# Kernel optimization log

Measured on AMD Instinct MI355X. Metric: run time of the kernel, lower is better.

Reference implementation:

```python
import jax, jax.numpy as jnp
import numpy as np

EPS = 1e-5

def bn(x, g, b, m, v):
    # inference-mode BatchNorm2d over channel dim
    return (x - m[None, :, None, None]) * jax.lax.rsqrt(v[None, :, None, None] + EPS) * g[None, :, None, None] + b[None, :, None, None]

def conv1x1(x, W, b=None):
    y = jnp.einsum('oc,bchw->bohw', W, x)
    return y + b[None, :, None, None] if b is not None else y

def forward(x, W3, b3, g1, b1, m1, v1, Wa, ba, g2, b2, m2, v2, Wq, bq, Wk, bk, Wv, bv, gam, Wg, bg, g3, b3n, m3, v3, Wf, bf, g4, b4, m4, v4, Wr, rs):
    B, C, H, Wd = x.shape
    N = H * Wd
    # conv branch: 3x3 conv + BN + ReLU
    y3 = jax.lax.conv_general_dilated(x, W3, (1, 1), ((1, 1), (1, 1)), dimension_numbers=('NCHW', 'OIHW', 'NCHW'))
    local = jax.nn.relu(bn(y3 + b3[None, :, None, None], g1, b1, m1, v1))
    # attn branch: 1x1 conv + BN + ReLU, then full-resolution attention
    a = jax.nn.relu(bn(conv1x1(x, Wa, ba), g2, b2, m2, v2))
    q = conv1x1(a, Wq, bq).reshape(B, -1, N)   # [B, C/8, N]
    k = conv1x1(a, Wk, bk).reshape(B, -1, N)   # [B, C/8, N]
    v = conv1x1(a, Wv, bv).reshape(B, -1, N)   # [B, C, N]
    att = jax.nn.softmax(jnp.einsum('bcn,bcm->bnm', q, k), axis=-1)  # [B, N, N], unscaled as in source
    o = jnp.einsum('bcm,bnm->bcn', v, att).reshape(a.shape)
    attn_feat = gam * o + a
    # gated fusion
    combined = jnp.concatenate([local, attn_feat], axis=1)
    gate = jax.nn.sigmoid(bn(conv1x1(combined, Wg, bg), g3, b3n, m3, v3))
    fused = gate * local + (1.0 - gate) * attn_feat
    out = jax.nn.relu(bn(conv1x1(jnp.concatenate([fused, combined], axis=1), Wf, bf), g4, b4, m4, v4))
    res = conv1x1(x, Wr)  # residual 1x1 conv, no bias (in != out channels)
    return out + rs * res

def setup_inputs() -> dict:
    B, Ci, Co, H, W_ = 4, 64, 128, 64, 64
    Cq = Co // 8
    ks = jax.random.split(jax.random.key(0), 24)
    def rn(i, s, sc=0.05):
        return jax.random.normal(ks[i], s, jnp.float32) * sc
    def var(i, c):
        return jax.random.uniform(ks[i], (c,), jnp.float32, 0.5, 1.5)
    ones = lambda c: jnp.ones((c,), jnp.float32)
    zeros = lambda c: jnp.zeros((c,), jnp.float32)
    return {
        'x': rn(0, (B, Ci, H, W_), 1.0),
        'W3': rn(1, (Co, Ci, 3, 3)), 'b3': rn(2, (Co,)),
        'g1': ones(Co), 'b1': zeros(Co), 'm1': rn(3, (Co,), 0.1), 'v1': var(4, Co),
        'Wa': rn(5, (Co, Ci)), 'ba': rn(6, (Co,)),
        'g2': ones(Co), 'b2': zeros(Co), 'm2': rn(7, (Co,), 0.1), 'v2': var(8, Co),
        'Wq': rn(9, (Cq, Co)), 'bq': rn(10, (Cq,)),
        'Wk': rn(11, (Cq, Co)), 'bk': rn(12, (Cq,)),
        'Wv': rn(13, (Co, Co)), 'bv': rn(14, (Co,)),
        'gam': jnp.array(0.5, jnp.float32),
        'Wg': rn(15, (Co, 2 * Co)), 'bg': rn(16, (Co,)),
        'g3': ones(Co), 'b3n': zeros(Co), 'm3': rn(17, (Co,), 0.1), 'v3': var(18, Co),
        'Wf': rn(19, (Co, 3 * Co)), 'bf': rn(20, (Co,)),
        'g4': ones(Co), 'b4': zeros(Co), 'm4': rn(21, (Co,), 0.1), 'v4': var(22, Co),
        'Wr': rn(23, (Co, Ci)),
        'rs': jnp.array(0.1, jnp.float32),
    }

def reference(x, W3, b3, g1, b1, m1, v1, Wa, ba, g2, b2, m2, v2, Wq, bq, Wk, bk, Wv, bv, gam, Wg, bg, g3, b3n, m3, v3, Wf, bf, g4, b4, m4, v4, Wr, rs):
    return forward(x, W3, b3, g1, b1, m1, v1, Wa, ba, g2, b2, m2, v2, Wq, bq, Wk, bk, Wv, bv, gam, Wg, bg, g3, b3n, m3, v3, Wf, bf, g4, b4, m4, v4, Wr, rs)
```

## Files before the change

### kernel.cpp

```cpp
#include <hip/hip_runtime.h>
#include <hip/hip_bf16.h>

#define CI_ 64
#define CO_ 128
#define NPIX 4096
#define CQ_ 16
#define EPS_ 1e-5f

typedef __attribute__((ext_vector_type(8))) __bf16 bf16x8;
typedef __attribute__((ext_vector_type(4))) __bf16 bf16x4;
typedef __attribute__((ext_vector_type(4))) float f32x4;

__global__ __launch_bounds__(256) void z_prepx(
    const float* __restrict__ x, __bf16* __restrict__ xT)
{
    __shared__ float tl[64][65];
    int b = blockIdx.x >> 6;
    int n0 = (blockIdx.x & 63) * 64;
    int tid = threadIdx.x;
    int nn = tid & 63, c4 = tid >> 6;
#pragma unroll
    for (int p = 0; p < 16; ++p) {
        int ci = p * 4 + c4;
        tl[ci][nn] = x[((size_t)b * CI_ + ci) * NPIX + n0 + nn];
    }
    __syncthreads();
#pragma unroll
    for (int p = 0; p < 2; ++p) {
        int idx = p * 256 + tid;
        int n = idx >> 3, cig = idx & 7;
        bf16x8 vv;
#pragma unroll
        for (int j = 0; j < 8; ++j) vv[j] = (__bf16)tl[cig * 8 + j][n];
        ((bf16x8*)xT)[((size_t)b * NPIX + n0 + n) * 8 + cig] = vv;
    }
}

__global__ __launch_bounds__(256) void z_prepw2(
    const float* __restrict__ W3, __bf16* __restrict__ Wt2,
    const float* __restrict__ Wg, const float* __restrict__ Wf, const float* __restrict__ Wr,
    const float* __restrict__ Wa, const float* __restrict__ Wq, const float* __restrict__ Wk,
    const float* __restrict__ Wv, __bf16* __restrict__ Wb)
{
    int i = blockIdx.x * 256 + threadIdx.x;
    if (i < 73728) {
        int co = i / 576;
        int r = i - co * 576;
        int tap = r >> 6;
        int ci = r & 63;
        Wt2[i] = (__bf16)W3[((size_t)co * CI_ + ci) * 9 + tap];
    }
    if (i < 118784) {
        float val;
        if (i < 32768) val = Wg[i];
        else if (i < 81920) val = Wf[i - 32768];
        else if (i < 90112) val = Wr[i - 81920];
        else if (i < 98304) val = Wa[i - 90112];
        else if (i < 100352) val = Wq[i - 98304];
        else if (i < 102400) val = Wk[i - 100352];
        else val = Wv[i - 102400];
        Wb[i] = (__bf16)val;
    }
}

__global__ __launch_bounds__(256) void z_mega(
    const __bf16* __restrict__ xT, const __bf16* __restrict__ Wb,
    const float* __restrict__ ba, const float* __restrict__ g2, const float* __restrict__ b2,
    const float* __restrict__ m2, const float* __restrict__ v2,
    const float* __restrict__ bq, const float* __restrict__ bk, const float* __restrict__ bv,
    float* __restrict__ a, float* __restrict__ q, __bf16* __restrict__ kT, __bf16* __restrict__ V2)
{
    __shared__ __align__(16) __bf16 an[16 * 128];
    int tid = threadIdx.x;
    int b = blockIdx.x >> 8;
    int n0 = (blockIdx.x & 255) * 16;
    int l = tid & 63, w = tid >> 6;
    int lm = l & 15, g = l >> 4;

    const __bf16* Wa2 = Wb + 90112;
    const __bf16* Wq2 = Wb + 98304;
    const __bf16* Wk2 = Wb + 100352;
    const __bf16* Wv2 = Wb + 102400;

    bf16x8 bx[2];
#pragma unroll
    for (int kc = 0; kc < 2; ++kc)
        bx[kc] = ((const bf16x8*)xT)[((size_t)b * NPIX + n0 + lm) * 8 + (kc * 4 + g)];
    f32x4 pa[2];
#pragma unroll
    for (int ct = 0; ct < 2; ++ct) {
#pragma unroll
        for (int r = 0; r < 4; ++r) pa[ct][r] = ba[w * 32 + ct * 16 + g * 4 + r];
#pragma unroll
        for (int kc = 0; kc < 2; ++kc) {
            bf16x8 afr = *(const bf16x8*)&Wa2[(size_t)(w * 32 + ct * 16 + lm) * 64 + kc * 32 + g * 8];
            pa[ct] = __builtin_amdgcn_mfma_f32_16x16x32_bf16(afr, bx[kc], pa[ct], 0, 0, 0);
        }
    }
#pragma unroll
    for (int ct = 0; ct < 2; ++ct) {
        bf16x4 pk;
#pragma unroll
        for (int r = 0; r < 4; ++r) {
            int co = w * 32 + ct * 16 + g * 4 + r;
            float sc = rsqrtf(v2[co] + EPS_) * g2[co];
            float sh = b2[co] - m2[co] * sc;
            float y = fmaxf(pa[ct][r] * sc + sh, 0.f);
            a[((size_t)b * CO_ + co) * NPIX + n0 + lm] = y;
            pk[r] = (__bf16)y;
        }
        int co8 = w * 4 + ct * 2 + (g >> 1);
        int ch = co8 ^ (lm & 7);
        *(bf16x4*)&an[lm * 128 + ch * 8 + (g & 1) * 4] = pk;
    }
    __syncthreads();

    bf16x8 bn[4];
#pragma unroll
    for (int kc = 0; kc < 4; ++kc) {
        int ch = (kc * 4 + g) ^ (lm & 7);
        bn[kc] = *(const bf16x8*)&an[lm * 128 + ch * 8];
    }
    f32x4 pv[2];
#pragma unroll
    for (int ct = 0; ct < 2; ++ct) {
#pragma unroll
        for (int r = 0; r < 4; ++r) pv[ct][r] = bv[w * 32 + ct * 16 + g * 4 + r];
#pragma unroll
        for (int kc = 0; kc < 4; ++kc) {
            bf16x8 afr = *(const bf16x8*)&Wv2[(size_t)(w * 32 + ct * 16 + lm) * 128 + kc * 32 + g * 8];
            pv[ct] = __builtin_amdgcn_mfma_f32_16x16x32_bf16(afr, bn[kc], pv[ct], 0, 0, 0);
        }
    }
    int n = n0 + lm;
#pragma unroll
    for (int ct = 0; ct < 2; ++ct)
#pragma unroll
        for (int r = 0; r < 4; ++r) {
            int c = w * 32 + ct * 16 + g * 4 + r;
            V2[(size_t)b * 524288 + (size_t)(n >> 3) * 1024 + c * 8 + (n & 7)] = (__bf16)pv[ct][r];
        }
    if (w == 0) {
        f32x4 pq;
#pragma unroll
        for (int r = 0; r < 4; ++r) pq[r] = bq[g * 4 + r];
#pragma unroll
        for (int kc = 0; kc < 4; ++kc) {
            bf16x8 afr = *(const bf16x8*)&Wq2[(size_t)lm * 128 + kc * 32 + g * 8];
            pq = __builtin_amdgcn_mfma_f32_16x16x32_bf16(afr, bn[kc], pq, 0, 0, 0);
        }
#pragma unroll
        for (int r = 0; r < 4; ++r)
            q[((size_t)b * CQ_ + g * 4 + r) * NPIX + n] = pq[r];
    } else if (w == 1) {
        f32x4 pk2;
#pragma unroll
        for (int r = 0; r < 4; ++r) pk2[r] = bk[g * 4 + r];
#pragma unroll
        for (int kc = 0; kc < 4; ++kc) {
            bf16x8 afr = *(const bf16x8*)&Wk2[(size_t)lm * 128 + kc * 32 + g * 8];
            pk2 = __builtin_amdgcn_mfma_f32_16x16x32_bf16(afr, bn[kc], pk2, 0, 0, 0);
        }
        bf16x4 kk;
#pragma unroll
        for (int r = 0; r < 4; ++r) kk[r] = (__bf16)pk2[r];
        *(bf16x4*)&kT[((size_t)b * NPIX + n) * CQ_ + g * 4] = kk;
    }
}

__global__ __launch_bounds__(256) void z_conv3m(
    const __bf16* __restrict__ xT, const __bf16* __restrict__ Wt2,
    const float* __restrict__ b3, const float* __restrict__ g,
    const float* __restrict__ bb, const float* __restrict__ m,
    const float* __restrict__ v, float* __restrict__ local)
{
    __shared__ __align__(16) __bf16 xt[3 * 66 * 64];
    __shared__ __align__(16) __bf16 wt[32 * 576];
    __shared__ float scs[32], shs[32];

    int blk = blockIdx.x;
    int b = blk >> 8;
    int h = (blk >> 2) & 63;
    int cg = blk & 3;
    int co0 = cg * 32;
    int tid = threadIdx.x;
    int l = tid & 63;
    int nt = tid >> 6;
    int lm = l & 15, lh = l >> 4;

    if (tid < 32) {
        int co = co0 + tid;
        float scv = rsqrtf(v[co] + EPS_) * g[co];
        scs[tid] = scv;
        shs[tid] = (b3[co] - m[co]) * scv + bb[co];
    }

    const bf16x8* xs = (const bf16x8*)xT + (size_t)b * (NPIX * 8);
    for (int i = tid; i < 1584; i += 256) {
        int r = i / 528;
        int rem = i - r * 528;
        int c = rem >> 3;
        int cig = rem & 7;
        int hh = h + r - 1;
        int gc = c - 1;
        bf16x8 val;
#pragma unroll
        for (int j = 0; j < 8; ++j) val[j] = (__bf16)0.f;
        if ((unsigned)hh < 64u && (unsigned)gc < 64u)
            val = xs[(hh * 64 + gc) * 8 + cig];
        *(bf16x8*)&xt[(r * 66 + c) * 64 + ((cig ^ (c & 7)) * 8)] = val;
    }
    const bf16x8* wsrc = (const bf16x8*)Wt2 + (size_t)co0 * 72;
    for (int i = tid; i < 2304; i += 256) {
        int co = i / 72;
        int kc = i - co * 72;
        *(bf16x8*)&wt[co * 576 + ((kc ^ (co & 7)) * 8)] = wsrc[i];
    }
    __syncthreads();

    f32x4 acc0 = {0.f, 0.f, 0.f, 0.f};
    f32x4 acc1 = {0.f, 0.f, 0.f, 0.f};
#pragma unroll
    for (int tap = 0; tap < 9; ++tap) {
        int dh = tap / 3, dw = tap % 3;
#pragma unroll
        for (int ks = 0; ks < 2; ++ks) {
            int cig = ks * 4 + lh;
            int col = nt * 16 + lm + dw;
            bf16x8 bfr = *(const bf16x8*)&xt[(dh * 66 + col) * 64 + ((cig ^ (col & 7)) * 8)];
            int kcg = tap * 8 + cig;
            bf16x8 a0 = *(const bf16x8*)&wt[lm * 576 + ((kcg ^ (lm & 7)) * 8)];
            bf16x8 a1 = *(const bf16x8*)&wt[(16 + lm) * 576 + ((kcg ^ (lm & 7)) * 8)];
            acc0 = __builtin_amdgcn_mfma_f32_16x16x32_bf16(a0, bfr, acc0, 0, 0, 0);
            acc1 = __builtin_amdgcn_mfma_f32_16x16x32_bf16(a1, bfr, acc1, 0, 0, 0);
        }
    }

    size_t obase = (size_t)b * CO_ * NPIX + h * 64 + nt * 16 + lm;
#pragma unroll
    for (int r = 0; r < 4; ++r) {
        int cl0 = lh * 4 + r;
        float y0 = fmaxf(acc0[r] * scs[cl0] + shs[cl0], 0.f);
        local[obase + (size_t)(co0 + cl0) * NPIX] = y0;
        int cl1 = 16 + cl0;
        float y1 = fmaxf(acc1[r] * scs[cl1] + shs[cl1], 0.f);
        local[obase + (size_t)(co0 + cl1) * NPIX] = y1;
    }
}

__global__ __launch_bounds__(256) void z_attn8(
    const float* __restrict__ q, const __bf16* __restrict__ kT, const __bf16* __restrict__ V2,
    __bf16* __restrict__ o_part, float2* __restrict__ ml)
{
    __shared__ __align__(16) unsigned char smem[16896];
    __shared__ float wmaxA[4][16], wsumA[4][16], fsA[16];
    __shared__ float wmaxB[4][16], wsumB[4][16], fsB[16];
    __bf16* pA = (__bf16*)smem;
    __bf16* pB = (__bf16*)(smem + 8448);
    float* o_lds = (float*)smem;

    int tid = threadIdx.x;
    int b = blockIdx.x >> 8;
    int half = (blockIdx.x >> 7) & 1;
    int q0 = (blockIdx.x & 127) * 32;
    int l = tid & 63;
    int w = tid >> 6;
    int lm = l & 15;
    int g = l >> 4;

    bf16x8 qfA, qfB;
#pragma unroll
    for (int j = 0; j < 8; ++j) { qfA[j] = (__bf16)0.f; qfB[j] = (__bf16)0.f; }
    if (g < 2) {
#pragma unroll
        for (int j = 0; j < 8; ++j) {
            qfA[j] = (__bf16)q[((size_t)b * CQ_ + g * 8 + j) * NPIX + q0 + lm];
            qfB[j] = (__bf16)q[((size_t)b * CQ_ + g * 8 + j) * NPIX + q0 + 16 + lm];
        }
    }

    float mA = -1e30f, lA = 0.f, mB = -1e30f, lB = 0.f;
    f32x4 aA0 = {0.f,0.f,0.f,0.f}, aA1 = {0.f,0.f,0.f,0.f};
    f32x4 aB0 = {0.f,0.f,0.f,0.f}, aB1 = {0.f,0.f,0.f,0.f};
    int c0 = w * 32 + lm;
    int c1 = c0 + 16;
    const bf16x8* vbase = (const bf16x8*)V2 + (size_t)b * 65536;
    const __bf16* ktb = kT + (size_t)b * NPIX * CQ_;

    for (int t = 0; t < 8; ++t) {
        int m0 = half * 2048 + t * 256;
        {
            f32x4 sfr[4];
#pragma unroll
            for (int ms = 0; ms < 4; ++ms) {
                bf16x8 kf;
#pragma unroll
                for (int j = 0; j < 8; ++j) kf[j] = (__bf16)0.f;
                if (g < 2)
                    kf = *(const bf16x8*)&ktb[(size_t)(m0 + w * 64 + ms * 16 + lm) * CQ_ + g * 8];
                f32x4 zz = {0.f, 0.f, 0.f, 0.f};
                sfr[ms] = __builtin_amdgcn_mfma_f32_16x16x32_bf16(kf, qfA, zz, 0, 0, 0);
            }
            float pmax = -1e30f;
#pragma unroll
            for (int ms = 0; ms < 4; ++ms)
#pragma unroll
                for (int r = 0; r < 4; ++r) pmax = fmaxf(pmax, sfr[ms][r]);
            pmax = fmaxf(pmax, __shfl_xor(pmax, 16));
            pmax = fmaxf(pmax, __shfl_xor(pmax, 32));
            if (g == 0) wmaxA[w][lm] = pmax;
            __syncthreads();
            float tmax = fmaxf(fmaxf(wmaxA[0][lm], wmaxA[1][lm]), fmaxf(wmaxA[2][lm], wmaxA[3][lm]));
            float nm = fmaxf(mA, tmax);
            float f = __expf(mA - nm);
            mA = nm;
            if (w == 0 && g == 0) fsA[lm] = f;
            float psum = 0.f;
#pragma unroll
            for (int ms = 0; ms < 4; ++ms) {
                float p0 = __expf(sfr[ms][0] - nm);
                float p1 = __expf(sfr[ms][1] - nm);
                float p2 = __expf(sfr[ms][2] - nm);
                float p3 = __expf(sfr[ms][3] - nm);
                psum += (p0 + p1) + (p2 + p3);
                bf16x4 pk;
                pk[0] = (__bf16)p0; pk[1] = (__bf16)p1; pk[2] = (__bf16)p2; pk[3] = (__bf16)p3;
                *(bf16x4*)&pA[lm * 264 + w * 64 + ms * 16 + g * 4] = pk;
            }
            psum += __shfl_xor(psum, 16);
            psum += __shfl_xor(psum, 32);
            if (g == 0) wsumA[w][lm] = psum;
            __syncthreads();
            float tsum = (wsumA[0][lm] + wsumA[1][lm]) + (wsumA[2][lm] + wsumA[3][lm]);
            lA = lA * f + tsum;
        }
        {
            f32x4 sfr[4];
#pragma unroll
            for (int ms = 0; ms < 4; ++ms) {
                bf16x8 kf;
#pragma unroll
                for (int j = 0; j < 8; ++j) kf[j] = (__bf16)0.f;
                if (g < 2)
                    kf = *(const bf16x8*)&ktb[(size_t)(m0 + w * 64 + ms * 16 + lm) * CQ_ + g * 8];
                f32x4 zz = {0.f, 0.f, 0.f, 0.f};
                sfr[ms] = __builtin_amdgcn_mfma_f32_16x16x32_bf16(kf, qfB, zz, 0, 0, 0);
            }
            float pmax = -1e30f;
#pragma unroll
            for (int ms = 0; ms < 4; ++ms)
#pragma unroll
                for (int r = 0; r < 4; ++r) pmax = fmaxf(pmax, sfr[ms][r]);
            pmax = fmaxf(pmax, __shfl_xor(pmax, 16));
            pmax = fmaxf(pmax, __shfl_xor(pmax, 32));
            if (g == 0) wmaxB[w][lm] = pmax;
            __syncthreads();
            float tmax = fmaxf(fmaxf(wmaxB[0][lm], wmaxB[1][lm]), fmaxf(wmaxB[2][lm], wmaxB[3][lm]));
            float nm = fmaxf(mB, tmax);
            float f = __expf(mB - nm);
            mB = nm;
            if (w == 0 && g == 0) fsB[lm] = f;
            float psum = 0.f;
#pragma unroll
            for (int ms = 0; ms < 4; ++ms) {
                float p0 = __expf(sfr[ms][0] - nm);
                float p1 = __expf(sfr[ms][1] - nm);
                float p2 = __expf(sfr[ms][2] - nm);
                float p3 = __expf(sfr[ms][3] - nm);
                psum += (p0 + p1) + (p2 + p3);
                bf16x4 pk;
                pk[0] = (__bf16)p0; pk[1] = (__bf16)p1; pk[2] = (__bf16)p2; pk[3] = (__bf16)p3;
                *(bf16x4*)&pB[lm * 264 + w * 64 + ms * 16 + g * 4] = pk;
            }
            psum += __shfl_xor(psum, 16);
            psum += __shfl_xor(psum, 32);
            if (g == 0) wsumB[w][lm] = psum;
            __syncthreads();
            float tsum = (wsumB[0][lm] + wsumB[1][lm]) + (wsumB[2][lm] + wsumB[3][lm]);
            lB = lB * f + tsum;
        }
        {
            float fA0 = fsA[g * 4 + 0], fA1 = fsA[g * 4 + 1], fA2 = fsA[g * 4 + 2], fA3 = fsA[g * 4 + 3];
            float fB0 = fsB[g * 4 + 0], fB1 = fsB[g * 4 + 1], fB2 = fsB[g * 4 + 2], fB3 = fsB[g * 4 + 3];
            aA0[0] *= fA0; aA0[1] *= fA1; aA0[2] *= fA2; aA0[3] *= fA3;
            aA1[0] *= fA0; aA1[1] *= fA1; aA1[2] *= fA2; aA1[3] *= fA3;
            aB0[0] *= fB0; aB0[1] *= fB1; aB0[2] *= fB2; aB0[3] *= fB3;
            aB1[0] *= fB0; aB1[1] *= fB1; aB1[2] *= fB2; aB1[3] *= fB3;
#pragma unroll
            for (int ks = 0; ks < 8; ++ks) {
                int msv = (m0 >> 3) + ks * 4 + g;
                bf16x8 bf0 = vbase[msv * 128 + c0];
                bf16x8 bf1 = vbase[msv * 128 + c1];
                bf16x8 afA = *(const bf16x8*)&pA[lm * 264 + ks * 32 + g * 8];
                bf16x8 afB = *(const bf16x8*)&pB[lm * 264 + ks * 32 + g * 8];
                aA0 = __builtin_amdgcn_mfma_f32_16x16x32_bf16(afA, bf0, aA0, 0, 0, 0);
                aA1 = __builtin_amdgcn_mfma_f32_16x16x32_bf16(afA, bf1, aA1, 0, 0, 0);
                aB0 = __builtin_amdgcn_mfma_f32_16x16x32_bf16(afB, bf0, aB0, 0, 0, 0);
                aB1 = __builtin_amdgcn_mfma_f32_16x16x32_bf16(afB, bf1, aB1, 0, 0, 0);
            }
        }
    }

    __syncthreads();
#pragma unroll
    for (int r = 0; r < 4; ++r) {
        int qrow = g * 4 + r;
        o_lds[c0 * 17 + qrow] = aA0[r];
        o_lds[c1 * 17 + qrow] = aA1[r];
    }
    if (w == 0 && g == 0)
        ml[(size_t)(half * 4 + b) * NPIX + q0 + lm] = make_float2(mA, lA);
    __syncthreads();
    {
        int qi = tid & 15;
        float inv = 1.f / lA;
#pragma unroll
        for (int j = 0; j < 8; ++j) {
            int cc = (tid >> 4) + 16 * j;
            size_t idx = ((size_t)(half * 4 + b) * CO_ + cc) * NPIX + q0 + qi;
            o_part[idx] = (__bf16)(o_lds[cc * 17 + qi] * inv);
        }
    }
    __syncthreads();
#pragma unroll
    for (int r = 0; r < 4; ++r) {
        int qrow = g * 4 + r;
        o_lds[c0 * 17 + qrow] = aB0[r];
        o_lds[c1 * 17 + qrow] = aB1[r];
    }
    if (w == 0 && g == 0)
        ml[(size_t)(half * 4 + b) * NPIX + q0 + 16 + lm] = make_float2(mB, lB);
    __syncthreads();
    {
        int qi = tid & 15;
        float inv = 1.f / lB;
#pragma unroll
        for (int j = 0; j < 8; ++j) {
            int cc = (tid >> 4) + 16 * j;
            size_t idx = ((size_t)(half * 4 + b) * CO_ + cc) * NPIX + q0 + 16 + qi;
            o_part[idx] = (__bf16)(o_lds[cc * 17 + qi] * inv);
        }
    }
}

__global__ __launch_bounds__(256) void z_acomb(
    const __bf16* __restrict__ o_part, const float2* __restrict__ ml,
    const float* __restrict__ a, const float* __restrict__ gamp, float* __restrict__ attn)
{
    int i = blockIdx.x * 256 + threadIdx.x;
    int n4 = (i & 1023) * 4;
    int co = (i >> 10) & (CO_ - 1);
    int b = i >> 17;
    float gam = gamp[0];
    bf16x4 o1 = *(const bf16x4*)&o_part[((size_t)b * CO_ + co) * NPIX + n4];
    bf16x4 o2 = *(const bf16x4*)&o_part[((size_t)(4 + b) * CO_ + co) * NPIX + n4];
    float4 av = *(const float4*)(a + ((size_t)b * CO_ + co) * NPIX + n4);
    float r[4], ai[4] = {av.x, av.y, av.z, av.w};
#pragma unroll
    for (int e = 0; e < 4; ++e) {
        float2 m1 = ml[(size_t)b * NPIX + n4 + e];
        float2 m2 = ml[(size_t)(4 + b) * NPIX + n4 + e];
        float mm = fmaxf(m1.x, m2.x);
        float w1 = m1.y * __expf(m1.x - mm);
        float w2 = m2.y * __expf(m2.x - mm);
        float o = ((float)o1[e] * w1 + (float)o2[e] * w2) / (w1 + w2);
        r[e] = gam * o + ai[e];
    }
    float4 rv = {r[0], r[1], r[2], r[3]};
    *(float4*)(attn + ((size_t)b * CO_ + co) * NPIX + n4) = rv;
}

__global__ __launch_bounds__(256) void z_fuseout2(
    const float* __restrict__ local, const float* __restrict__ attn, const float* __restrict__ x,
    const __bf16* __restrict__ Wb,
    const float* __restrict__ bg, const float* __restrict__ g3, const float* __restrict__ b3n,
    const float* __restrict__ m3, const float* __restrict__ v3,
    const float* __restrict__ bfb, const float* __restrict__ g4, const float* __restrict__ b4,
    const float* __restrict__ m4, const float* __restrict__ v4,
    const float* __restrict__ rsp, float* __restrict__ out)
{
    __shared__ __align__(16) unsigned char smem[32768 + 4096];
    __bf16* sb2 = (__bf16*)smem;
    __bf16* sxT = (__bf16*)(smem + 28672);

    int tid = threadIdx.x;
    int b = blockIdx.x >> 7;
    int n0 = (blockIdx.x & 127) * 32;

#pragma unroll
    for (int p = 0; p < 4; ++p) {
        int idx = p * 256 + tid;
        int c = idx >> 3, j = idx & 7;
        float lv[4], av[4];
        *(float4*)lv = *(const float4*)(local + ((size_t)b * CO_ + c) * NPIX + n0 + j * 4);
        *(float4*)av = *(const float4*)(attn + ((size_t)b * CO_ + c) * NPIX + n0 + j * 4);
#pragma unroll
        for (int e = 0; e < 4; ++e) {
            int n = j * 4 + e;
            int k1 = 128 + c, k2 = 256 + c;
            sb2[n * 448 + (((k1 >> 3) ^ (n & 7)) << 3) + (k1 & 7)] = (__bf16)lv[e];
            sb2[n * 448 + (((k2 >> 3) ^ (n & 7)) << 3) + (k2 & 7)] = (__bf16)av[e];
        }
    }
#pragma unroll
    for (int p = 0; p < 2; ++p) {
        int idx = p * 256 + tid;
        int c = idx >> 3, j = idx & 7;
        float xv[4];
        *(float4*)xv = *(const float4*)(x + ((size_t)b * CI_ + c) * NPIX + n0 + j * 4);
#pragma unroll
        for (int e = 0; e < 4; ++e) {
            int n = j * 4 + e;
            sxT[n * 64 + (((c >> 3) ^ (n & 7)) << 3) + (c & 7)] = (__bf16)xv[e];
        }
    }
    __syncthreads();

    int l = tid & 63, w = tid >> 6;
    int lm = l & 15, g = l >> 4;
    int co0 = w * 32;
    int t7 = lm & 7;

    f32x4 p1[2][2];
#pragma unroll
    for (int cs = 0; cs < 2; ++cs) {
        float bv = bg[co0 + cs * 16 + lm];
#pragma unroll
        for (int ns = 0; ns < 2; ++ns) {
            p1[ns][cs][0] = bv; p1[ns][cs][1] = bv; p1[ns][cs][2] = bv; p1[ns][cs][3] = bv;
        }
    }
    const __bf16* Wg2 = Wb;
#pragma unroll
    for (int kc = 0; kc < 8; ++kc) {
        int ch = (16 + kc * 4 + g) ^ t7;
        bf16x8 a0 = *(const bf16x8*)&sb2[lm * 448 + ch * 8];
        bf16x8 a1 = *(const bf16x8*)&sb2[(16 + lm) * 448 + ch * 8];
        bf16x8 b0 = *(const bf16x8*)&Wg2[(size_t)(co0 + lm) * 256 + kc * 32 + g * 8];
        bf16x8 b1 = *(const bf16x8*)&Wg2[(size_t)(co0 + 16 + lm) * 256 + kc * 32 + g * 8];
        p1[0][0] = __builtin_amdgcn_mfma_f32_16x16x32_bf16(a0, b0, p1[0][0], 0, 0, 0);
        p1[0][1] = __builtin_amdgcn_mfma_f32_16x16x32_bf16(a0, b1, p1[0][1], 0, 0, 0);
        p1[1][0] = __builtin_amdgcn_mfma_f32_16x16x32_bf16(a1, b0, p1[1][0], 0, 0, 0);
        p1[1][1] = __builtin_amdgcn_mfma_f32_16x16x32_bf16(a1, b1, p1[1][1], 0, 0, 0);
    }
#pragma unroll
    for (int cs = 0; cs < 2; ++cs) {
        int co = co0 + cs * 16 + lm;
        float sc3 = rsqrtf(v3[co] + EPS_) * g3[co];
        float sh3 = b3n[co] - m3[co] * sc3;
        int kl = 128 + co, ka = 256 + co;
#pragma unroll
        for (int ns = 0; ns < 2; ++ns)
#pragma unroll
            for (int r = 0; r < 4; ++r) {
                int n = ns * 16 + g * 4 + r;
                float z = p1[ns][cs][r] * sc3 + sh3;
                float gate = 1.f / (1.f + __expf(-z));
                float lv = (float)sb2[n * 448 + (((kl >> 3) ^ (n & 7)) << 3) + (kl & 7)];
                float av = (float)sb2[n * 448 + (((ka >> 3) ^ (n & 7)) << 3) + (ka & 7)];
                float fu = gate * lv + (1.f - gate) * av;
                sb2[n * 448 + (((co >> 3) ^ (n & 7)) << 3) + (co & 7)] = (__bf16)fu;
            }
    }
    __syncthreads();

    f32x4 p2[2][2], pr[2][2];
#pragma unroll
    for (int cs = 0; cs < 2; ++cs) {
        float bv = bfb[co0 + cs * 16 + lm];
#pragma unroll
        for (int ns = 0; ns < 2; ++ns) {
            p2[ns][cs][0] = bv; p2[ns][cs][1] = bv; p2[ns][cs][2] = bv; p2[ns][cs][3] = bv;
            pr[ns][cs] = (f32x4){0.f, 0.f, 0.f, 0.f};
        }
    }
    const __bf16* Wf2 = Wb + 32768;
    const __bf16* Wr2 = Wb + 81920;
#pragma unroll
    for (int kc = 0; kc < 12; ++kc) {
        int ch = (kc * 4 + g) ^ t7;
        bf16x8 a0 = *(const bf16x8*)&sb2[lm * 448 + ch * 8];
        bf16x8 a1 = *(const bf16x8*)&sb2[(16 + lm) * 448 + ch * 8];
        bf16x8 b0 = *(const bf16x8*)&Wf2[(size_t)(co0 + lm) * 384 + kc * 32 + g * 8];
        bf16x8 b1 = *(const bf16x8*)&Wf2[(size_t)(co0 + 16 + lm) * 384 + kc * 32 + g * 8];
        p2[0][0] = __builtin_amdgcn_mfma_f32_16x16x32_bf16(a0, b0, p2[0][0], 0, 0, 0);
        p2[0][1] = __builtin_amdgcn_mfma_f32_16x16x32_bf16(a0, b1, p2[0][1], 0, 0, 0);
        p2[1][0] = __builtin_amdgcn_mfma_f32_16x16x32_bf16(a1, b0, p2[1][0], 0, 0, 0);
        p2[1][1] = __builtin_amdgcn_mfma_f32_16x16x32_bf16(a1, b1, p2[1][1], 0, 0, 0);
    }
#pragma unroll
    for (int kc = 0; kc < 2; ++kc) {
        int ch = (kc * 4 + g) ^ t7;
        bf16x8 a0 = *(const bf16x8*)&sxT[lm * 64 + ch * 8];
        bf16x8 a1 = *(const bf16x8*)&sxT[(16 + lm) * 64 + ch * 8];
        bf16x8 b0 = *(const bf16x8*)&Wr2[(size_t)(co0 + lm) * 64 + kc * 32 + g * 8];
        bf16x8 b1 = *(const bf16x8*)&Wr2[(size_t)(co0 + 16 + lm) * 64 + kc * 32 + g * 8];
        pr[0][0] = __builtin_amdgcn_mfma_f32_16x16x32_bf16(a0, b0, pr[0][0], 0, 0, 0);
        pr[0][1] = __builtin_amdgcn_mfma_f32_16x16x32_bf16(a0, b1, pr[0][1], 0, 0, 0);
        pr[1][0] = __builtin_amdgcn_mfma_f32_16x16x32_bf16(a1, b0, pr[1][0], 0, 0, 0);
        pr[1][1] = __builtin_amdgcn_mfma_f32_16x16x32_bf16(a1, b1, pr[1][1], 0, 0, 0);
    }
    __syncthreads();

    float* o_lds = (float*)smem;
    float rsv = rsp[0];
#pragma unroll
    for (int cs = 0; cs < 2; ++cs) {
        int co = co0 + cs * 16 + lm;
        float sc4 = rsqrtf(v4[co] + EPS_) * g4[co];
        float sh4 = b4[co] - m4[co] * sc4;
#pragma unroll
        for (int ns = 0; ns < 2; ++ns)
#pragma unroll
            for (int r = 0; r < 4; ++r) {
                int n = ns * 16 + g * 4 + r;
                float o = fmaxf(p2[ns][cs][r] * sc4 + sh4, 0.f) + rsv * pr[ns][cs][r];
                o_lds[co * 36 + n] = o;
            }
    }
    __syncthreads();
    {
        int c = tid >> 1, h = tid & 1;
#pragma unroll
        for (int j2 = 0; j2 < 4; ++j2) {
            float4 vv = *(float4*)&o_lds[c * 36 + h * 16 + j2 * 4];
            *(float4*)(out + ((size_t)b * CO_ + c) * NPIX + n0 + h * 16 + j2 * 4) = vv;
        }
    }
}

extern "C" void kernel_launch(void* const* d_in, const int* in_sizes, int n_in,
                              void* d_out, int out_size, void* d_ws, size_t ws_size,
                              hipStream_t stream) {
    const float* x   = (const float*)d_in[0];
    const float* W3  = (const float*)d_in[1];
    const float* b3  = (const float*)d_in[2];
    const float* g1  = (const float*)d_in[3];
    const float* b1  = (const float*)d_in[4];
    const float* m1  = (const float*)d_in[5];
    const float* v1  = (const float*)d_in[6];
    const float* Wa  = (const float*)d_in[7];
    const float* ba  = (const float*)d_in[8];
    const float* g2  = (const float*)d_in[9];
    const float* b2  = (const float*)d_in[10];
    const float* m2  = (const float*)d_in[11];
    const float* v2  = (const float*)d_in[12];
    const float* Wq  = (const float*)d_in[13];
    const float* bq  = (const float*)d_in[14];
    const float* Wk  = (const float*)d_in[15];
    const float* bk  = (const float*)d_in[16];
    const float* Wv  = (const float*)d_in[17];
    const float* bv  = (const float*)d_in[18];
    const float* gam = (const float*)d_in[19];
    const float* Wg  = (const float*)d_in[20];
    const float* bg  = (const float*)d_in[21];
    const float* g3  = (const float*)d_in[22];
    const float* b3n = (const float*)d_in[23];
    const float* m3  = (const float*)d_in[24];
    const float* v3  = (const float*)d_in[25];
    const float* Wf  = (const float*)d_in[26];
    const float* bfb = (const float*)d_in[27];
    const float* g4  = (const float*)d_in[28];
    const float* b4  = (const float*)d_in[29];
    const float* m4  = (const float*)d_in[30];
    const float* v4  = (const float*)d_in[31];
    const float* Wr  = (const float*)d_in[32];
    const float* rs  = (const float*)d_in[33];

    float* ws    = (float*)d_ws;
    float* a_    = ws;
    float* local = ws + 2097152;
    float* attn  = ws + 4194304;
    __bf16* V2   = (__bf16*)(ws + 6291456);
    float* q     = ws + 7340032;
    __bf16* kT   = (__bf16*)(ws + 7602176);
    __bf16* xT   = (__bf16*)(ws + 7864320);
    __bf16* Wt2  = (__bf16*)(ws + 8388608);
    __bf16* Wb   = (__bf16*)(ws + 8450048);
    __bf16* o_part = (__bf16*)(ws + 8509440);
    float2* ml   = (float2*)(ws + 10606592);

    float* out = (float*)d_out;

    z_prepx<<<256, 256, 0, stream>>>(x, xT);
    z_prepw2<<<464, 256, 0, stream>>>(W3, Wt2, Wg, Wf, Wr, Wa, Wq, Wk, Wv, Wb);
    z_mega<<<1024, 256, 0, stream>>>(xT, Wb, ba, g2, b2, m2, v2, bq, bk, bv, a_, q, kT, V2);
    z_attn8<<<1024, 256, 0, stream>>>(q, kT, V2, o_part, ml);
    z_acomb<<<2048, 256, 0, stream>>>(o_part, ml, a_, gam, attn);
    z_conv3m<<<1024, 256, 0, stream>>>(xT, Wt2, b3, g1, b1, m1, v1, local);
    z_fuseout2<<<512, 256, 0, stream>>>(local, attn, x, Wb, bg, g3, b3n, m3, v3,
                                        bfb, g4, b4, m4, v4, rs, out);
}
```

Measured before the change: 112.8 us.

## Fuse attention combine into fusion kernel and store conv branch in bf16

Removes the separate z_acomb kernel: the split-softmax merge of the two attention halves and the gamma*o + a residual are now done inside the fusion kernel as it stages its tiles. The 3x3 conv branch writes its output as bf16 instead of fp32, and the fusion kernel reads the precomputed bf16 transposed x instead of re-transposing fp32 x. This removes one launch and the fp32 attn/local intermediate round trips through memory. It adds rounding of local to bf16 before storage, which the old path already applied when staging into shared memory.

After: 109.6 us. 1.03x faster.

```diff
diff --git a/kernel.cpp b/kernel.cpp
--- a/kernel.cpp
+++ b/kernel.cpp
@@ -168,11 +168,11 @@
     }
 }
 
-__global__ __launch_bounds__(256) void z_conv3m(
+__global__ __launch_bounds__(256) void z_conv3mb(
     const __bf16* __restrict__ xT, const __bf16* __restrict__ Wt2,
     const float* __restrict__ b3, const float* __restrict__ g,
     const float* __restrict__ bb, const float* __restrict__ m,
-    const float* __restrict__ v, float* __restrict__ local)
+    const float* __restrict__ v, __bf16* __restrict__ local_bf)
 {
     __shared__ __align__(16) __bf16 xt[3 * 66 * 64];
     __shared__ __align__(16) __bf16 wt[32 * 576];
@@ -241,10 +241,10 @@
     for (int r = 0; r < 4; ++r) {
         int cl0 = lh * 4 + r;
         float y0 = fmaxf(acc0[r] * scs[cl0] + shs[cl0], 0.f);
-        local[obase + (size_t)(co0 + cl0) * NPIX] = y0;
+        local_bf[obase + (size_t)(co0 + cl0) * NPIX] = (__bf16)y0;
         int cl1 = 16 + cl0;
         float y1 = fmaxf(acc1[r] * scs[cl1] + shs[cl1], 0.f);
-        local[obase + (size_t)(co0 + cl1) * NPIX] = y1;
+        local_bf[obase + (size_t)(co0 + cl1) * NPIX] = (__bf16)y1;
     }
 }
 
@@ -443,35 +443,10 @@
     }
 }
 
-__global__ __launch_bounds__(256) void z_acomb(
-    const __bf16* __restrict__ o_part, const float2* __restrict__ ml,
-    const float* __restrict__ a, const float* __restrict__ gamp, float* __restrict__ attn)
-{
-    int i = blockIdx.x * 256 + threadIdx.x;
-    int n4 = (i & 1023) * 4;
-    int co = (i >> 10) & (CO_ - 1);
-    int b = i >> 17;
-    float gam = gamp[0];
-    bf16x4 o1 = *(const bf16x4*)&o_part[((size_t)b * CO_ + co) * NPIX + n4];
-    bf16x4 o2 = *(const bf16x4*)&o_part[((size_t)(4 + b) * CO_ + co) * NPIX + n4];
-    float4 av = *(const float4*)(a + ((size_t)b * CO_ + co) * NPIX + n4);
-    float r[4], ai[4] = {av.x, av.y, av.z, av.w};
-#pragma unroll
-    for (int e = 0; e < 4; ++e) {
-        float2 m1 = ml[(size_t)b * NPIX + n4 + e];
-        float2 m2 = ml[(size_t)(4 + b) * NPIX + n4 + e];
-        float mm = fmaxf(m1.x, m2.x);
-        float w1 = m1.y * __expf(m1.x - mm);
-        float w2 = m2.y * __expf(m2.x - mm);
-        float o = ((float)o1[e] * w1 + (float)o2[e] * w2) / (w1 + w2);
-        r[e] = gam * o + ai[e];
-    }
-    float4 rv = {r[0], r[1], r[2], r[3]};
-    *(float4*)(attn + ((size_t)b * CO_ + co) * NPIX + n4) = rv;
-}
-
-__global__ __launch_bounds__(256) void z_fuseout2(
-    const float* __restrict__ local, const float* __restrict__ attn, const float* __restrict__ x,
+__global__ __launch_bounds__(256) void z_fuseout3(
+    const __bf16* __restrict__ local_bf, const __bf16* __restrict__ o_part,
+    const float2* __restrict__ ml, const float* __restrict__ a,
+    const float* __restrict__ gamp, const __bf16* __restrict__ xT,
     const __bf16* __restrict__ Wb,
     const float* __restrict__ bg, const float* __restrict__ g3, const float* __restrict__ b3n,
     const float* __restrict__ m3, const float* __restrict__ v3,
@@ -480,6 +455,7 @@
     const float* __restrict__ rsp, float* __restrict__ out)
 {
     __shared__ __align__(16) unsigned char smem[32768 + 4096];
+    __shared__ float wA[32], wB[32];
     __bf16* sb2 = (__bf16*)smem;
     __bf16* sxT = (__bf16*)(smem + 28672);
 
@@ -487,32 +463,43 @@
     int b = blockIdx.x >> 7;
     int n0 = (blockIdx.x & 127) * 32;
 
+    if (tid < 32) {
+        float2 m1 = ml[(size_t)b * NPIX + n0 + tid];
+        float2 m2 = ml[(size_t)(4 + b) * NPIX + n0 + tid];
+        float mm = fmaxf(m1.x, m2.x);
+        float w1 = m1.y * __expf(m1.x - mm);
+        float w2 = m2.y * __expf(m2.x - mm);
+        float inv = 1.f / (w1 + w2);
+        wA[tid] = w1 * inv;
+        wB[tid] = w2 * inv;
+    }
+    __syncthreads();
+
+    float gam = gamp[0];
 #pragma unroll
     for (int p = 0; p < 4; ++p) {
         int idx = p * 256 + tid;
         int c = idx >> 3, j = idx & 7;
-        float lv[4], av[4];
-        *(float4*)lv = *(const float4*)(local + ((size_t)b * CO_ + c) * NPIX + n0 + j * 4);
-        *(float4*)av = *(const float4*)(attn + ((size_t)b * CO_ + c) * NPIX + n0 + j * 4);
+        bf16x4 lv = *(const bf16x4*)&local_bf[((size_t)b * CO_ + c) * NPIX + n0 + j * 4];
+        bf16x4 o1 = *(const bf16x4*)&o_part[((size_t)b * CO_ + c) * NPIX + n0 + j * 4];
+        bf16x4 o2 = *(const bf16x4*)&o_part[((size_t)(4 + b) * CO_ + c) * NPIX + n0 + j * 4];
+        float av[4];
+        *(float4*)av = *(const float4*)(a + ((size_t)b * CO_ + c) * NPIX + n0 + j * 4);
 #pragma unroll
         for (int e = 0; e < 4; ++e) {
             int n = j * 4 + e;
             int k1 = 128 + c, k2 = 256 + c;
-            sb2[n * 448 + (((k1 >> 3) ^ (n & 7)) << 3) + (k1 & 7)] = (__bf16)lv[e];
-            sb2[n * 448 + (((k2 >> 3) ^ (n & 7)) << 3) + (k2 & 7)] = (__bf16)av[e];
+            sb2[n * 448 + (((k1 >> 3) ^ (n & 7)) << 3) + (k1 & 7)] = lv[e];
+            float o = (float)o1[e] * wA[n] + (float)o2[e] * wB[n];
+            sb2[n * 448 + (((k2 >> 3) ^ (n & 7)) << 3) + (k2 & 7)] = (__bf16)(gam * o + av[e]);
         }
     }
 #pragma unroll
     for (int p = 0; p < 2; ++p) {
         int idx = p * 256 + tid;
-        int c = idx >> 3, j = idx & 7;
-        float xv[4];
-        *(float4*)xv = *(const float4*)(x + ((size_t)b * CI_ + c) * NPIX + n0 + j * 4);
-#pragma unroll
-        for (int e = 0; e < 4; ++e) {
-            int n = j * 4 + e;
-            sxT[n * 64 + (((c >> 3) ^ (n & 7)) << 3) + (c & 7)] = (__bf16)xv[e];
-        }
+        int n = idx >> 3, cig = idx & 7;
+        bf16x8 vv = ((const bf16x8*)xT)[((size_t)b * NPIX + n0 + n) * 8 + cig];
+        *(bf16x8*)&sxT[n * 64 + ((cig ^ (n & 7)) << 3)] = vv;
     }
     __syncthreads();
 
@@ -667,18 +654,17 @@
     const float* Wr  = (const float*)d_in[32];
     const float* rs  = (const float*)d_in[33];
 
-    float* ws    = (float*)d_ws;
-    float* a_    = ws;
-    float* local = ws + 2097152;
-    float* attn  = ws + 4194304;
-    __bf16* V2   = (__bf16*)(ws + 6291456);
-    float* q     = ws + 7340032;
-    __bf16* kT   = (__bf16*)(ws + 7602176);
-    __bf16* xT   = (__bf16*)(ws + 7864320);
-    __bf16* Wt2  = (__bf16*)(ws + 8388608);
-    __bf16* Wb   = (__bf16*)(ws + 8450048);
-    __bf16* o_part = (__bf16*)(ws + 8509440);
-    float2* ml   = (float2*)(ws + 10606592);
+    float* ws      = (float*)d_ws;
+    float* a_      = ws;
+    __bf16* local_bf = (__bf16*)(ws + 2097152);
+    __bf16* V2     = (__bf16*)(ws + 3145728);
+    float* q       = ws + 4194304;
+    __bf16* kT     = (__bf16*)(ws + 4456448);
+    __bf16* xT     = (__bf16*)(ws + 4587520);
+    __bf16* Wt2    = (__bf16*)(ws + 5111808);
+    __bf16* Wb     = (__bf16*)(ws + 5152768);
+    __bf16* o_part = (__bf16*)(ws + 5214208);
+    float2* ml     = (float2*)(ws + 7311360);
 
     float* out = (float*)d_out;
 
@@ -686,8 +672,7 @@
     z_prepw2<<<464, 256, 0, stream>>>(W3, Wt2, Wg, Wf, Wr, Wa, Wq, Wk, Wv, Wb);
     z_mega<<<1024, 256, 0, stream>>>(xT, Wb, ba, g2, b2, m2, v2, bq, bk, bv, a_, q, kT, V2);
     z_attn8<<<1024, 256, 0, stream>>>(q, kT, V2, o_part, ml);
-    z_acomb<<<2048, 256, 0, stream>>>(o_part, ml, a_, gam, attn);
-    z_conv3m<<<1024, 256, 0, stream>>>(xT, Wt2, b3, g1, b1, m1, v1, local);
-    z_fuseout2<<<512, 256, 0, stream>>>(local, attn, x, Wb, bg, g3, b3n, m3, v3,
-                                        bfb, g4, b4, m4, v4, rs, out);
+    z_conv3mb<<<1024, 256, 0, stream>>>(xT, Wt2, b3, g1, b1, m1, v1, local_bf);
+    z_fuseout3<<<512, 256, 0, stream>>>(local_bf, o_part, ml, a_, gam, xT, Wb,
+                                        bg, g3, b3n, m3, v3, bfb, g4, b4, m4, v4, rs, out);
 }
```
